# Kernel optimization log

Measured on AMD Instinct MI355X. Metric: run time of the kernel, lower is better.

The kernel has to match this reference:

```python
import jax, jax.numpy as jnp
import numpy as np

B, N, D, KD = 8, 2048, 64, 64

def setup_inputs() -> dict:
    key = jax.random.key(0)
    ks = jax.random.split(key, 7)
    s = 1.0 / np.sqrt(D)
    return {
        "x":  jax.random.normal(ks[0], (B, N, D), dtype=jnp.float32),
        "Wq": jax.random.normal(ks[1], (D, KD), dtype=jnp.float32) * s,
        "bq": jnp.zeros((KD,), jnp.float32),
        "Wk": jax.random.normal(ks[2], (D, KD), dtype=jnp.float32) * s,
        "bk": jnp.zeros((KD,), jnp.float32),
        "Wv": jax.random.normal(ks[3], (D, KD), dtype=jnp.float32) * s,
        "bv": jnp.zeros((KD,), jnp.float32),
    }

def reference(x, Wq, bq, Wk, bk, Wv, bv):
    # Q,K,V: [B,N,KD]
    Q = x @ Wq + bq
    K = x @ Wk + bk
    V = x @ Wv + bv
    # scores: [B,N,N] (note: original applies NO 1/sqrt(d) scaling)
    scores = jnp.einsum('bij,bkj->bik', Q, K)
    probs = jax.nn.softmax(scores, axis=-1)
    # mean-threshold sparsification: keep entries above the row mean
    mask = (probs > jnp.mean(probs, axis=-1, keepdims=True)).astype(probs.dtype)
    sparse = probs * mask
    out = jnp.einsum('bij,bjk->bik', sparse, V)  # [B,N,KD]
    return out
```

## Files before the change

kernel.cpp:

```cpp
#include <hip/hip_runtime.h>

#define NB 8
#define NS 2048
#define ND 64
#define LOG2E 1.44269504f

typedef _Float16 half8 __attribute__((ext_vector_type(8)));
typedef __attribute__((ext_vector_type(4))) float floatx4;

__device__ __forceinline__ half8 cvt8(const float* p) {
    float4 a = *(const float4*)p;
    float4 b = *(const float4*)(p + 4);
    half8 h = {(_Float16)a.x, (_Float16)a.y, (_Float16)a.z, (_Float16)a.w,
               (_Float16)b.x, (_Float16)b.y, (_Float16)b.z, (_Float16)b.w};
    return h;
}
__device__ __forceinline__ half8 cvtWcol(const float* base) {
    half8 h;
#pragma unroll
    for (int j = 0; j < 8; ++j) h[j] = (_Float16)base[j * 64];
    return h;
}

__global__ __launch_bounds__(256) void qkv_proj(
    const float* __restrict__ x,
    const float* __restrict__ Wq, const float* __restrict__ bq,
    const float* __restrict__ Wk, const float* __restrict__ bk,
    const float* __restrict__ Wv, const float* __restrict__ bv,
    _Float16* __restrict__ Qg, _Float16* __restrict__ Kg,
    _Float16* __restrict__ Vt)
{
    __shared__ _Float16 vt[64 * 18];

    const int tid  = threadIdx.x;
    const int wv   = tid >> 6;
    const int l    = tid & 63;
    const int quad = l >> 4;
    const int tx   = l & 15;

    const int b  = blockIdx.x & 7;
    const int n0 = (blockIdx.x >> 3) * 16;

    const float* xr = x + ((size_t)b * NS + n0 + tx) * ND + quad * 8;
    half8 a0 = cvt8(xr);
    half8 a1 = cvt8(xr + 32);

    const floatx4 zf = {0.f, 0.f, 0.f, 0.f};

#pragma unroll
    for (int i = 0; i < 3; ++i) {
        const int ct = wv * 3 + i;
        const int m  = ct >> 2;
        const int lcol = (ct & 3) * 16 + tx;

        const float* Wm;
        const float* Bm;
        if (m == 0)      { Wm = Wq; Bm = bq; }
        else if (m == 1) { Wm = Wk; Bm = bk; }
        else             { Wm = Wv; Bm = bv; }

        half8 b0 = cvtWcol(Wm + (quad * 8) * 64 + lcol);
        half8 b1 = cvtWcol(Wm + (32 + quad * 8) * 64 + lcol);

        floatx4 acc = __builtin_amdgcn_mfma_f32_16x16x32_f16(a0, b0, zf, 0, 0, 0);
        acc = __builtin_amdgcn_mfma_f32_16x16x32_f16(a1, b1, acc, 0, 0, 0);
        const float bias = Bm[lcol];

        if (m == 0) {
#pragma unroll
            for (int r = 0; r < 4; ++r)
                Qg[((size_t)b * NS + n0 + quad * 4 + r) * ND + lcol] =
                    (_Float16)((acc[r] + bias) * LOG2E);
        } else if (m == 1) {
#pragma unroll
            for (int r = 0; r < 4; ++r)
                Kg[((size_t)b * NS + n0 + quad * 4 + r) * ND + lcol] = (_Float16)(acc[r] + bias);
        } else {
#pragma unroll
            for (int r = 0; r < 4; ++r)
                vt[lcol * 18 + quad * 4 + r] = (_Float16)(acc[r] + bias);
        }
    }
    __syncthreads();
    {
        const int d = tid >> 2, seg = tid & 3;
        uint2 p = *(uint2*)&vt[d * 18 + seg * 4];
        *(uint2*)(Vt + ((size_t)b * ND + d) * NS + n0 + seg * 4) = p;
    }
}

__global__ __launch_bounds__(512, 2) void attn(
    const _Float16* __restrict__ Qg,
    const _Float16* __restrict__ Kg,
    const _Float16* __restrict__ Vt,
    float* __restrict__ out)
{
    __shared__ _Float16 ksm[2 * 64 * 72];
    __shared__ _Float16 vsm[2 * 64 * 72];
    __shared__ _Float16 psm[64 * 72];
    __shared__ float lsh[256];

    const int tid  = threadIdx.x;
    const int wv   = tid >> 6;
    const int l    = tid & 63;
    const int quad = l >> 4;
    const int tx   = l & 15;
    const int h    = wv >> 2;
    const int kq   = wv & 3;

    const int b  = blockIdx.x & 7;
    const int q0 = (blockIdx.x >> 3) * 64;

    const _Float16* Qb = Qg + ((size_t)b * NS + q0 + h * 32) * ND;
    const _Float16* Kb = Kg + (size_t)b * NS * ND;
    const _Float16* Vb = Vt + (size_t)b * ND * NS;

    half8 qf[2][2];
#pragma unroll
    for (int rt = 0; rt < 2; ++rt)
#pragma unroll
        for (int kc = 0; kc < 2; ++kc)
            qf[rt][kc] = *(const half8*)(Qb + (size_t)(rt * 16 + tx) * ND + kc * 32 + quad * 8);

    const int skey = tid >> 3;
    const int sc   = (tid & 7) * 8;
    const _Float16* Ksrc = Kb + (size_t)skey * ND + sc;
    const _Float16* Vsrc = Vb + (size_t)skey * NS + sc;
    const int sdst = skey * 72 + sc;

    const floatx4 zf = {0.f, 0.f, 0.f, 0.f};
    const int krow = (kq * 16 + tx) * 72;

    float lacc[2][4] = {{0.f,0.f,0.f,0.f},{0.f,0.f,0.f,0.f}};
    {
        uint4 gk = *(const uint4*)Ksrc;
        *(uint4*)(ksm + sdst) = gk;
        for (int t = 0; t < 32; ++t) {
            const int buf = (t & 1) * 4608;
            __syncthreads();
            if (t < 31) gk = *(const uint4*)(Ksrc + (size_t)(t + 1) * 64 * ND);
            half8 kf0 = *(const half8*)(ksm + buf + krow + quad * 8);
            half8 kf1 = *(const half8*)(ksm + buf + krow + 32 + quad * 8);
#pragma unroll
            for (int rt = 0; rt < 2; ++rt) {
                floatx4 c = __builtin_amdgcn_mfma_f32_16x16x32_f16(qf[rt][0], kf0, zf, 0, 0, 0);
                c = __builtin_amdgcn_mfma_f32_16x16x32_f16(qf[rt][1], kf1, c, 0, 0, 0);
#pragma unroll
                for (int r = 0; r < 4; ++r)
                    lacc[rt][r] += __builtin_amdgcn_exp2f(c[r]);
            }
            if (t < 31) *(uint4*)(ksm + (buf ^ 4608) + sdst) = gk;
        }
    }
#pragma unroll
    for (int off = 1; off < 16; off <<= 1)
#pragma unroll
        for (int rt = 0; rt < 2; ++rt)
#pragma unroll
            for (int r = 0; r < 4; ++r)
                lacc[rt][r] += __shfl_xor(lacc[rt][r], off);
    if (tx == 0) {
#pragma unroll
        for (int rt = 0; rt < 2; ++rt)
#pragma unroll
            for (int r = 0; r < 4; ++r)
                lsh[kq * 64 + h * 32 + rt * 16 + quad * 4 + r] = lacc[rt][r];
    }

    uint4 gk2 = *(const uint4*)Ksrc;
    uint4 gv  = *(const uint4*)Vsrc;
    __syncthreads();

    float inv[2][4], thr[2][4];
#pragma unroll
    for (int rt = 0; rt < 2; ++rt)
#pragma unroll
        for (int r = 0; r < 4; ++r) {
            const int row = h * 32 + rt * 16 + quad * 4 + r;
            float L = lsh[row] + lsh[64 + row] + lsh[128 + row] + lsh[192 + row];
            inv[rt][r] = 1.f / L;
            thr[rt][r] = L * (1.f / (float)NS);
        }

    *(uint4*)(ksm + sdst) = gk2;
    *(uint4*)(vsm + sdst) = gv;
    floatx4 o[2] = {zf, zf};

    for (int t = 0; t < 32; ++t) {
        const int buf = (t & 1) * 4608;
        __syncthreads();
        if (t < 31) {
            gk2 = *(const uint4*)(Ksrc + (size_t)(t + 1) * 64 * ND);
            gv  = *(const uint4*)(Vsrc + (size_t)(t + 1) * 64);
        }
        half8 kf0 = *(const half8*)(ksm + buf + krow + quad * 8);
        half8 kf1 = *(const half8*)(ksm + buf + krow + 32 + quad * 8);
#pragma unroll
        for (int rt = 0; rt < 2; ++rt) {
            floatx4 c = __builtin_amdgcn_mfma_f32_16x16x32_f16(qf[rt][0], kf0, zf, 0, 0, 0);
            c = __builtin_amdgcn_mfma_f32_16x16x32_f16(qf[rt][1], kf1, c, 0, 0, 0);
#pragma unroll
            for (int r = 0; r < 4; ++r) {
                float e = __builtin_amdgcn_exp2f(c[r]);
                float w = (e > thr[rt][r]) ? e * inv[rt][r] : 0.f;
                psm[(h * 32 + rt * 16 + quad * 4 + r) * 72 + kq * 16 + tx] = (_Float16)w;
            }
        }
        __syncthreads();
#pragma unroll
        for (int ck = 0; ck < 2; ++ck) {
            half8 vf = *(const half8*)(vsm + buf + krow + ck * 32 + quad * 8);
#pragma unroll
            for (int rt = 0; rt < 2; ++rt) {
                half8 af = *(const half8*)(psm + (h * 32 + rt * 16 + tx) * 72 + ck * 32 + quad * 8);
                o[rt] = __builtin_amdgcn_mfma_f32_16x16x32_f16(af, vf, o[rt], 0, 0, 0);
            }
        }
        if (t < 31) {
            *(uint4*)(ksm + (buf ^ 4608) + sdst) = gk2;
            *(uint4*)(vsm + (buf ^ 4608) + sdst) = gv;
        }
    }

#pragma unroll
    for (int rt = 0; rt < 2; ++rt)
#pragma unroll
        for (int r = 0; r < 4; ++r)
            out[((size_t)b * NS + q0 + h * 32 + rt * 16 + quad * 4 + r) * ND + kq * 16 + tx] =
                o[rt][r];
}

extern "C" void kernel_launch(void* const* d_in, const int* in_sizes, int n_in,
                              void* d_out, int out_size, void* d_ws, size_t ws_size,
                              hipStream_t stream) {
    const float* x  = (const float*)d_in[0];
    const float* Wq = (const float*)d_in[1];
    const float* bq = (const float*)d_in[2];
    const float* Wk = (const float*)d_in[3];
    const float* bk = (const float*)d_in[4];
    const float* Wv = (const float*)d_in[5];
    const float* bv = (const float*)d_in[6];

    _Float16* Qg = (_Float16*)d_ws;
    _Float16* Kg = Qg + (size_t)NB * NS * ND;
    _Float16* Vt = Kg + (size_t)NB * NS * ND;

    qkv_proj<<<NB * (NS / 16), 256, 0, stream>>>(x, Wq, bq, Wk, bk, Wv, bv, Qg, Kg, Vt);
    attn<<<NB * (NS / 64), 512, 0, stream>>>(Qg, Kg, Vt, (float*)d_out);
}
```

Measured before the change: 107.8 us.

## Cache quantized int16 scores in global memory instead of recomputing QK^T

The first pass now quantizes each log2-domain score to int16 (scale 256) and writes it to a workspace buffer while summing exponentials. The second pass reads those codes back instead of recomputing Q·K^T. It rebuilds the normalized probabilities with exp2(code/256 - log2 L) and applies the mean threshold as a cutoff at -11 in log2 space. The PV stage is also reorganized to split the key dimension across the four kq waves, with a serialized shared-memory reduction at the end. This trades the second QK matmul and its K reloads for about 64 MB each of global writes and reads. It also adds quantization error and a larger workspace requirement.

```diff
diff --git a/kernel.cpp b/kernel.cpp
--- a/kernel.cpp
+++ b/kernel.cpp
@@ -4,8 +4,11 @@
 #define NS 2048
 #define ND 64
 #define LOG2E 1.44269504f
+#define QSC 256.0f
+#define IQS (1.0f / 256.0f)
 
 typedef _Float16 half8 __attribute__((ext_vector_type(8)));
+typedef short short8 __attribute__((ext_vector_type(8)));
 typedef __attribute__((ext_vector_type(4))) float floatx4;
 
 __device__ __forceinline__ half8 cvt8(const float* p) {
@@ -93,12 +96,11 @@
     const _Float16* __restrict__ Qg,
     const _Float16* __restrict__ Kg,
     const _Float16* __restrict__ Vt,
+    short* __restrict__ ct,
     float* __restrict__ out)
 {
-    __shared__ _Float16 ksm[2 * 64 * 72];
-    __shared__ _Float16 vsm[2 * 64 * 72];
-    __shared__ _Float16 psm[64 * 72];
-    __shared__ float lsh[256];
+    __shared__ __align__(16) _Float16 smem[2 * 64 * 136];
+    __shared__ float lsh[4 * 64];
 
     const int tid  = threadIdx.x;
     const int wv   = tid >> 6;
@@ -114,120 +116,174 @@
     const _Float16* Qb = Qg + ((size_t)b * NS + q0 + h * 32) * ND;
     const _Float16* Kb = Kg + (size_t)b * NS * ND;
     const _Float16* Vb = Vt + (size_t)b * ND * NS;
+    short* ctb = ct + ((size_t)b * NS + q0) * NS;
 
     half8 qf[2][2];
 #pragma unroll
-    for (int rt = 0; rt < 2; ++rt)
+    for (int rh = 0; rh < 2; ++rh)
 #pragma unroll
         for (int kc = 0; kc < 2; ++kc)
-            qf[rt][kc] = *(const half8*)(Qb + (size_t)(rt * 16 + tx) * ND + kc * 32 + quad * 8);
-
-    const int skey = tid >> 3;
-    const int sc   = (tid & 7) * 8;
-    const _Float16* Ksrc = Kb + (size_t)skey * ND + sc;
-    const _Float16* Vsrc = Vb + (size_t)skey * NS + sc;
-    const int sdst = skey * 72 + sc;
+            qf[rh][kc] = *(const half8*)(Qb + (size_t)(rh * 16 + tx) * ND + kc * 32 + quad * 8);
 
     const floatx4 zf = {0.f, 0.f, 0.f, 0.f};
-    const int krow = (kq * 16 + tx) * 72;
-
-    float lacc[2][4] = {{0.f,0.f,0.f,0.f},{0.f,0.f,0.f,0.f}};
+
     {
+        const int skey = tid >> 3;
+        const int sc   = (tid & 7) * 8;
+        const _Float16* Ksrc = Kb + (size_t)skey * ND + sc;
+        const int sdst = skey * 72 + sc;
+        const int krow = (kq * 16 + tx) * 72;
+
+        short* cst0 = ctb + (size_t)(h * 32 + tx) * NS + kq * 16 + quad * 4;
+        short* cst1 = cst0 + (size_t)16 * NS;
+
+        float lacc0 = 0.f, lacc1 = 0.f;
+
         uint4 gk = *(const uint4*)Ksrc;
-        *(uint4*)(ksm + sdst) = gk;
+        *(uint4*)(smem + sdst) = gk;
         for (int t = 0; t < 32; ++t) {
             const int buf = (t & 1) * 4608;
             __syncthreads();
             if (t < 31) gk = *(const uint4*)(Ksrc + (size_t)(t + 1) * 64 * ND);
-            half8 kf0 = *(const half8*)(ksm + buf + krow + quad * 8);
-            half8 kf1 = *(const half8*)(ksm + buf + krow + 32 + quad * 8);
-#pragma unroll
-            for (int rt = 0; rt < 2; ++rt) {
-                floatx4 c = __builtin_amdgcn_mfma_f32_16x16x32_f16(qf[rt][0], kf0, zf, 0, 0, 0);
-                c = __builtin_amdgcn_mfma_f32_16x16x32_f16(qf[rt][1], kf1, c, 0, 0, 0);
+            half8 kf0 = *(const half8*)(smem + buf + krow + quad * 8);
+            half8 kf1 = *(const half8*)(smem + buf + krow + 32 + quad * 8);
+#pragma unroll
+            for (int rh = 0; rh < 2; ++rh) {
+                floatx4 c = __builtin_amdgcn_mfma_f32_16x16x32_f16(kf0, qf[rh][0], zf, 0, 0, 0);
+                c = __builtin_amdgcn_mfma_f32_16x16x32_f16(kf1, qf[rh][1], c, 0, 0, 0);
+                int ci[4];
+                float ladd = 0.f;
+#pragma unroll
+                for (int r = 0; r < 4; ++r) {
+                    float cs = fminf(fmaxf(c[r] * QSC, -32767.f), 32767.f);
+                    int ic = (int)rintf(cs);
+                    ci[r] = ic;
+                    ladd += __builtin_amdgcn_exp2f((float)ic * IQS);
+                }
+                if (rh == 0) lacc0 += ladd; else lacc1 += ladd;
+                uint2 pk;
+                pk.x = (unsigned)(ci[0] & 0xffff) | ((unsigned)(ci[1] & 0xffff) << 16);
+                pk.y = (unsigned)(ci[2] & 0xffff) | ((unsigned)(ci[3] & 0xffff) << 16);
+                *(uint2*)((rh ? cst1 : cst0) + (size_t)t * 64) = pk;
+            }
+            if (t < 31) *(uint4*)(smem + (buf ^ 4608) + sdst) = gk;
+        }
+
+#pragma unroll
+        for (int off = 16; off < 64; off <<= 1) {
+            lacc0 += __shfl_xor(lacc0, off);
+            lacc1 += __shfl_xor(lacc1, off);
+        }
+        if (quad == 0) {
+            lsh[kq * 64 + h * 32 + tx]      = lacc0;
+            lsh[kq * 64 + h * 32 + 16 + tx] = lacc1;
+        }
+    }
+
+    const int sdim = tid >> 4;
+    const int sseg = (tid & 15) * 8;
+    const _Float16* Vsrc0 = Vb + (size_t)sdim * NS + sseg;
+    const _Float16* Vsrc1 = Vb + (size_t)(sdim + 32) * NS + sseg;
+    const int vdst0 = sdim * 136 + sseg;
+    const int vdst1 = (sdim + 32) * 136 + sseg;
+
+    const short* crd0 = ctb + (size_t)(h * 32 + tx) * NS + kq * 32 + quad * 8;
+    const short* crd1 = crd0 + (size_t)16 * NS;
+
+    uint4 gv0 = *(const uint4*)Vsrc0;
+    uint4 gv1 = *(const uint4*)Vsrc1;
+    short8 ca0 = *(const short8*)crd0;
+    short8 ca1 = *(const short8*)crd1;
+
+    __syncthreads();
+
+    float lg2L0, lg2L1;
+    {
+        const int row = h * 32 + tx;
+        float L0 = lsh[row] + lsh[64 + row] + lsh[128 + row] + lsh[192 + row];
+        float L1 = lsh[row + 16] + lsh[64 + row + 16] + lsh[128 + row + 16] + lsh[192 + row + 16];
+        lg2L0 = __builtin_amdgcn_logf(L0);
+        lg2L1 = __builtin_amdgcn_logf(L1);
+    }
+
+    *(uint4*)(smem + vdst0) = gv0;
+    *(uint4*)(smem + vdst1) = gv1;
+
+    floatx4 o[2][4] = {{zf, zf, zf, zf}, {zf, zf, zf, zf}};
+
+    for (int t = 0; t < 16; ++t) {
+        const int buf = (t & 1) * 8704;
+        __syncthreads();
+        short8 cn0, cn1;
+        if (t < 15) {
+            gv0 = *(const uint4*)(Vsrc0 + (size_t)(t + 1) * 128);
+            gv1 = *(const uint4*)(Vsrc1 + (size_t)(t + 1) * 128);
+            cn0 = *(const short8*)(crd0 + (size_t)(t + 1) * 128);
+            cn1 = *(const short8*)(crd1 + (size_t)(t + 1) * 128);
+        }
+        half8 a0, a1;
+#pragma unroll
+        for (int j = 0; j < 8; ++j) {
+            float d0 = (float)ca0[j] * IQS - lg2L0;
+            a0[j] = (d0 > -11.f) ? (_Float16)__builtin_amdgcn_exp2f(d0) : (_Float16)0.f;
+            float d1 = (float)ca1[j] * IQS - lg2L1;
+            a1[j] = (d1 > -11.f) ? (_Float16)__builtin_amdgcn_exp2f(d1) : (_Float16)0.f;
+        }
+#pragma unroll
+        for (int dg = 0; dg < 4; ++dg) {
+            half8 vf = *(const half8*)(smem + buf + (dg * 16 + tx) * 136 + kq * 32 + quad * 8);
+            o[0][dg] = __builtin_amdgcn_mfma_f32_16x16x32_f16(a0, vf, o[0][dg], 0, 0, 0);
+            o[1][dg] = __builtin_amdgcn_mfma_f32_16x16x32_f16(a1, vf, o[1][dg], 0, 0, 0);
+        }
+        if (t < 15) {
+            *(uint4*)(smem + (buf ^ 8704) + vdst0) = gv0;
+            *(uint4*)(smem + (buf ^ 8704) + vdst1) = gv1;
+            ca0 = cn0; ca1 = cn1;
+        }
+    }
+
+    __syncthreads();
+    float* osm = (float*)smem;
+    if (kq == 0) {
+#pragma unroll
+        for (int rt = 0; rt < 2; ++rt)
+#pragma unroll
+            for (int dg = 0; dg < 4; ++dg)
 #pragma unroll
                 for (int r = 0; r < 4; ++r)
-                    lacc[rt][r] += __builtin_amdgcn_exp2f(c[r]);
-            }
-            if (t < 31) *(uint4*)(ksm + (buf ^ 4608) + sdst) = gk;
-        }
-    }
-#pragma unroll
-    for (int off = 1; off < 16; off <<= 1)
+                    osm[(h * 32 + rt * 16 + quad * 4 + r) * 68 + dg * 16 + tx] = o[rt][dg][r];
+    }
+    __syncthreads();
+    if (kq == 1) {
 #pragma unroll
         for (int rt = 0; rt < 2; ++rt)
 #pragma unroll
-            for (int r = 0; r < 4; ++r)
-                lacc[rt][r] += __shfl_xor(lacc[rt][r], off);
-    if (tx == 0) {
+            for (int dg = 0; dg < 4; ++dg)
+#pragma unroll
+                for (int r = 0; r < 4; ++r)
+                    osm[(h * 32 + rt * 16 + quad * 4 + r) * 68 + dg * 16 + tx] += o[rt][dg][r];
+    }
+    __syncthreads();
+    if (kq == 2) {
 #pragma unroll
         for (int rt = 0; rt < 2; ++rt)
 #pragma unroll
-            for (int r = 0; r < 4; ++r)
-                lsh[kq * 64 + h * 32 + rt * 16 + quad * 4 + r] = lacc[rt][r];
-    }
-
-    uint4 gk2 = *(const uint4*)Ksrc;
-    uint4 gv  = *(const uint4*)Vsrc;
-    __syncthreads();
-
-    float inv[2][4], thr[2][4];
-#pragma unroll
-    for (int rt = 0; rt < 2; ++rt)
-#pragma unroll
-        for (int r = 0; r < 4; ++r) {
-            const int row = h * 32 + rt * 16 + quad * 4 + r;
-            float L = lsh[row] + lsh[64 + row] + lsh[128 + row] + lsh[192 + row];
-            inv[rt][r] = 1.f / L;
-            thr[rt][r] = L * (1.f / (float)NS);
-        }
-
-    *(uint4*)(ksm + sdst) = gk2;
-    *(uint4*)(vsm + sdst) = gv;
-    floatx4 o[2] = {zf, zf};
-
-    for (int t = 0; t < 32; ++t) {
-        const int buf = (t & 1) * 4608;
-        __syncthreads();
-        if (t < 31) {
-            gk2 = *(const uint4*)(Ksrc + (size_t)(t + 1) * 64 * ND);
-            gv  = *(const uint4*)(Vsrc + (size_t)(t + 1) * 64);
-        }
-        half8 kf0 = *(const half8*)(ksm + buf + krow + quad * 8);
-        half8 kf1 = *(const half8*)(ksm + buf + krow + 32 + quad * 8);
-#pragma unroll
-        for (int rt = 0; rt < 2; ++rt) {
-            floatx4 c = __builtin_amdgcn_mfma_f32_16x16x32_f16(qf[rt][0], kf0, zf, 0, 0, 0);
-            c = __builtin_amdgcn_mfma_f32_16x16x32_f16(qf[rt][1], kf1, c, 0, 0, 0);
-#pragma unroll
-            for (int r = 0; r < 4; ++r) {
-                float e = __builtin_amdgcn_exp2f(c[r]);
-                float w = (e > thr[rt][r]) ? e * inv[rt][r] : 0.f;
-                psm[(h * 32 + rt * 16 + quad * 4 + r) * 72 + kq * 16 + tx] = (_Float16)w;
-            }
-        }
-        __syncthreads();
-#pragma unroll
-        for (int ck = 0; ck < 2; ++ck) {
-            half8 vf = *(const half8*)(vsm + buf + krow + ck * 32 + quad * 8);
-#pragma unroll
-            for (int rt = 0; rt < 2; ++rt) {
-                half8 af = *(const half8*)(psm + (h * 32 + rt * 16 + tx) * 72 + ck * 32 + quad * 8);
-                o[rt] = __builtin_amdgcn_mfma_f32_16x16x32_f16(af, vf, o[rt], 0, 0, 0);
-            }
-        }
-        if (t < 31) {
-            *(uint4*)(ksm + (buf ^ 4608) + sdst) = gk2;
-            *(uint4*)(vsm + (buf ^ 4608) + sdst) = gv;
-        }
-    }
-
-#pragma unroll
-    for (int rt = 0; rt < 2; ++rt)
-#pragma unroll
-        for (int r = 0; r < 4; ++r)
-            out[((size_t)b * NS + q0 + h * 32 + rt * 16 + quad * 4 + r) * ND + kq * 16 + tx] =
-                o[rt][r];
+            for (int dg = 0; dg < 4; ++dg)
+#pragma unroll
+                for (int r = 0; r < 4; ++r)
+                    osm[(h * 32 + rt * 16 + quad * 4 + r) * 68 + dg * 16 + tx] += o[rt][dg][r];
+    }
+    __syncthreads();
+    if (kq == 3) {
+#pragma unroll
+        for (int rt = 0; rt < 2; ++rt)
+#pragma unroll
+            for (int dg = 0; dg < 4; ++dg)
+#pragma unroll
+                for (int r = 0; r < 4; ++r)
+                    out[((size_t)b * NS + q0 + h * 32 + rt * 16 + quad * 4 + r) * ND + dg * 16 + tx] =
+                        osm[(h * 32 + rt * 16 + quad * 4 + r) * 68 + dg * 16 + tx] + o[rt][dg][r];
+    }
 }
 
 extern "C" void kernel_launch(void* const* d_in, const int* in_sizes, int n_in,
@@ -244,7 +300,8 @@
     _Float16* Qg = (_Float16*)d_ws;
     _Float16* Kg = Qg + (size_t)NB * NS * ND;
     _Float16* Vt = Kg + (size_t)NB * NS * ND;
+    short*    ct = (short*)(Vt + (size_t)NB * NS * ND);
 
     qkv_proj<<<NB * (NS / 16), 256, 0, stream>>>(x, Wq, bq, Wk, bk, Wv, bv, Qg, Kg, Vt);
-    attn<<<NB * (NS / 64), 512, 0, stream>>>(Qg, Kg, Vt, (float*)d_out);
-}
+    attn<<<NB * (NS / 64), 512, 0, stream>>>(Qg, Kg, Vt, ct, (float*)d_out);
+}
```

Result: slower. 122.8 us (+13.8%).
